# Kernel optimization log

Measured on AMD Instinct MI355X. Metric: run time of the kernel, lower is better.

## Reference

```python
import jax, jax.numpy as jnp
import numpy as np

NUM_CLASSES = 4
SMOOTH = 1e-05
W_DICE, W_CE, W_BOUND = 1.0, 1.0, 0.01
BIG = 1e8  # effectively-infinite squared distance


def _edt_sq_pass(f, axis):
    # Exact 1D squared-distance transform along `axis` via min-plus:
    # out[i] = min_j f[j] + (i-j)^2  (brute-force O(n^2), fully vectorized)
    n = f.shape[axis]
    i = jnp.arange(n, dtype=f.dtype)
    d2 = (i[:, None] - i[None, :]) ** 2  # [n, n]
    fm = jnp.moveaxis(f, axis, -1)
    out = jnp.min(fm[..., None, :] + d2, axis=-1)
    return jnp.moveaxis(out, -1, axis)


def _edt(zero_mask):
    # Euclidean distance to the nearest True voxel of zero_mask
    # (equivalent to scipy distance_transform_edt(~zero_mask)'s convention:
    #  distance to nearest zero of the input == nearest True of zero_mask).
    f = jnp.where(zero_mask, 0.0, BIG).astype(jnp.float32)
    for ax in range(f.ndim):
        f = _edt_sq_pass(f, ax)
    return jnp.sqrt(f)


def _signed_distance(mask):
    # mask: bool [D,H,W]; signed distance map: + outside, - inside.
    d_out = _edt(mask)            # distance(1 - mask)
    d_in = _edt(~mask)            # distance(mask)
    sdf = d_out - d_in
    total = jnp.sum(mask)
    size = mask.size
    sdf = jnp.where(total == 0, jnp.ones_like(sdf), sdf)
    sdf = jnp.where(total == size, -jnp.ones_like(sdf), sdf)
    return sdf


def setup_inputs() -> dict:
    key = jax.random.key(0)
    k1, k2 = jax.random.split(key)
    preds = jax.random.normal(k1, (4, NUM_CLASSES, 64, 64, 64), dtype=jnp.float32)
    targets = jax.random.randint(k2, (4, 64, 64, 64), 0, NUM_CLASSES, dtype=jnp.int32)
    return {"preds": preds, "targets": targets}


def reference(preds, targets):
    B = preds.shape[0]
    probs = jax.nn.softmax(preds, axis=1)  # [B,C,D,H,W]

    # --- Soft Dice ---
    onehot = jax.nn.one_hot(targets, NUM_CLASSES, dtype=preds.dtype)  # [B,D,H,W,C]
    onehot = jnp.moveaxis(onehot, -1, 1)  # [B,C,D,H,W]
    inter = jnp.sum(probs * onehot, axis=(2, 3, 4))
    union = jnp.sum(probs, axis=(2, 3, 4)) + jnp.sum(onehot, axis=(2, 3, 4))
    dice = (2.0 * inter + SMOOTH) / (union + SMOOTH)
    l_dice = 1.0 - jnp.mean(dice)

    # --- Cross entropy (mean over all voxels) ---
    logp = jax.nn.log_softmax(preds, axis=1)
    picked = jnp.take_along_axis(logp, targets[:, None].astype(jnp.int32), axis=1)
    l_ce = -jnp.mean(picked)

    # --- Boundary loss (classes 1..C-1) ---
    l_bound = jnp.float32(0.0)
    for c in range(1, NUM_CLASSES):
        mask_c = targets == c  # [B,D,H,W]
        sdf_c = jax.vmap(_signed_distance)(mask_c)  # [B,D,H,W]
        l_bound = l_bound + jnp.sum(jnp.mean(sdf_c * probs[:, c], axis=(1, 2, 3)))
    l_bound = l_bound / (B * (NUM_CLASSES - 1))

    return W_DICE * l_dice + W_CE * l_ce + W_BOUND * l_bound
```

## Files before the change

### kernel.cpp

```cpp
#include <hip/hip_runtime.h>
#include <hip/hip_bf16.h>
#include <math.h>

#define NVOX 262144
#define BIGF 1e8f
#define GRID_B 768
#define GRID_K2 768

__device__ __forceinline__ unsigned short f2bf(float x) {
    __hip_bfloat16 h = __float2bfloat16(x);
    return *reinterpret_cast<unsigned short*>(&h);
}
__device__ __forceinline__ float bf2f(unsigned short u) {
    __hip_bfloat16 h = *reinterpret_cast<__hip_bfloat16*>(&u);
    return __bfloat162float(h);
}
__device__ __forceinline__ unsigned short dist2_u16(unsigned long long mask, int w) {
    if (mask == 0ull) return 0xFFFFu;
    unsigned long long mr = mask >> w;
    unsigned long long ml = mask << (63 - w);
    int dr = mr ? __builtin_ctzll(mr) : 127;
    int dl = ml ? __builtin_clzll(ml) : 127;
    int dd = dr < dl ? dr : dl;
    return (unsigned short)(dd * dd);
}

__global__ __launch_bounds__(256) void kA_probs(
    const float* __restrict__ preds, unsigned short* __restrict__ probsT) {
    int bid = blockIdx.x, t = threadIdx.x;
    int g0 = bid * 1024 + 4 * t;
    int b = g0 >> 18;
    int v0 = g0 & (NVOX - 1);
    const float* p = preds + (size_t)(b * 4) * NVOX + v0;
    float4 x0 = *(const float4*)(p);
    float4 x1 = *(const float4*)(p + NVOX);
    float4 x2 = *(const float4*)(p + 2 * NVOX);
    float4 x3 = *(const float4*)(p + 3 * NVOX);

    const float L2E = 1.4426950408889634f;
    unsigned short pb[3][4];
    #pragma unroll
    for (int j = 0; j < 4; ++j) {
        float a0 = (&x0.x)[j], a1 = (&x1.x)[j], a2 = (&x2.x)[j], a3 = (&x3.x)[j];
        float m  = fmaxf(fmaxf(a0, a1), fmaxf(a2, a3));
        float e0 = exp2f((a0 - m) * L2E);
        float e1 = exp2f((a1 - m) * L2E);
        float e2 = exp2f((a2 - m) * L2E);
        float e3 = exp2f((a3 - m) * L2E);
        float inv = __builtin_amdgcn_rcpf(e0 + e1 + e2 + e3);
        pb[0][j] = f2bf(e1 * inv);
        pb[1][j] = f2bf(e2 * inv);
        pb[2][j] = f2bf(e3 * inv);
    }
    int d = v0 >> 12, h = (v0 >> 6) & 63, w0 = v0 & 63;
    size_t poff = (size_t)h * 4096 + d * 64 + w0;
    #pragma unroll
    for (int c = 0; c < 3; ++c) {
        ushort4 u = make_ushort4(pb[c][0], pb[c][1], pb[c][2], pb[c][3]);
        *(ushort4*)(probsT + (size_t)(b * 3 + c) * NVOX + poff) = u;
    }
}

__global__ __launch_bounds__(256) void kA_stats(
    const float* __restrict__ preds, const int* __restrict__ targets,
    float* __restrict__ part_stats) {
    __shared__ float sred[4 * 13];
    int bid = blockIdx.x, t = threadIdx.x, lane = t & 63, wid = t >> 6;
    int g0 = bid * 1024 + 4 * t;
    int b = g0 >> 18;
    int v0 = g0 & (NVOX - 1);
    const float* p = preds + (size_t)(b * 4) * NVOX + v0;
    float4 x0 = *(const float4*)(p);
    float4 x1 = *(const float4*)(p + NVOX);
    float4 x2 = *(const float4*)(p + 2 * NVOX);
    float4 x3 = *(const float4*)(p + 3 * NVOX);
    int4 tv4 = *(const int4*)(targets + (size_t)b * NVOX + v0);

    const float L2E = 1.4426950408889634f;
    const float LN2 = 0.6931471805599453f;
    float q[13];
    #pragma unroll
    for (int k = 0; k < 13; ++k) q[k] = 0.0f;

    #pragma unroll
    for (int j = 0; j < 4; ++j) {
        float a0 = (&x0.x)[j], a1 = (&x1.x)[j], a2 = (&x2.x)[j], a3 = (&x3.x)[j];
        int tv = (&tv4.x)[j];
        float m  = fmaxf(fmaxf(a0, a1), fmaxf(a2, a3));
        float e0 = exp2f((a0 - m) * L2E);
        float e1 = exp2f((a1 - m) * L2E);
        float e2 = exp2f((a2 - m) * L2E);
        float e3 = exp2f((a3 - m) * L2E);
        float ssum = e0 + e1 + e2 + e3;
        float inv  = __builtin_amdgcn_rcpf(ssum);
        float p0 = e0 * inv, p1 = e1 * inv, p2 = e2 * inv, p3 = e3 * inv;
        float xt = (tv == 0) ? a0 : (tv == 1) ? a1 : (tv == 2) ? a2 : a3;
        q[12] += (m - xt) + log2f(ssum) * LN2;
        q[4] += p0; q[5] += p1; q[6] += p2; q[7] += p3;
        if (tv == 0)      { q[0] += p0; q[8]  += 1.0f; }
        else if (tv == 1) { q[1] += p1; q[9]  += 1.0f; }
        else if (tv == 2) { q[2] += p2; q[10] += 1.0f; }
        else              { q[3] += p3; q[11] += 1.0f; }
    }

    #pragma unroll
    for (int k = 0; k < 13; ++k) {
        float x = q[k];
        #pragma unroll
        for (int o = 32; o > 0; o >>= 1) x += __shfl_down(x, o);
        if (lane == 0) sred[wid * 13 + k] = x;
    }
    __syncthreads();
    if (t < 13) {
        float s = sred[t] + sred[13 + t] + sred[26 + t] + sred[39 + t];
        part_stats[t * 1024 + bid] = s;
    }
}

__global__ __launch_bounds__(256) void kB_edt12(
    const int* __restrict__ targets, unsigned short* __restrict__ bufA) {
    __shared__ unsigned short tO[64 * 66];
    __shared__ unsigned short tI[64 * 66];
    int blk = blockIdx.x;
    int cm = blk % 3;
    int bd = blk / 3;
    int d = bd & 63, b = bd >> 6;
    int c = cm + 1;
    int t = threadIdx.x, lane = t & 63, wid = t >> 6;
    const int* tg = targets + (size_t)b * NVOX + (size_t)d * 4096;

    #pragma unroll
    for (int i = 0; i < 16; ++i) {
        int e = t + 256 * i;
        int h = wid + 4 * i;
        int tv = tg[e];
        unsigned long long mask = __ballot(tv == c);
        tO[h * 66 + lane] = dist2_u16(mask, lane);
        tI[h * 66 + lane] = dist2_u16(~mask, lane);
    }
    __syncthreads();

    for (int r = 0; r < 16; ++r) {
        int w = wid * 16 + r;
        {
            float best = (float)tO[lane * 66 + w];
            for (int dk = 1; dk < 64; ++dk) {
                float d2 = (float)(dk * dk);
                if (__all(d2 >= best)) break;
                int hl = lane - dk; hl = hl < 0 ? 0 : hl;
                int hr = lane + dk; hr = hr > 63 ? 63 : hr;
                best = fminf(fminf(best, (float)tO[hl * 66 + w] + d2),
                             (float)tO[hr * 66 + w] + d2);
            }
            tO[lane * 66 + w] = (unsigned short)best;
        }
        {
            float best = (float)tI[lane * 66 + w];
            for (int dk = 1; dk < 64; ++dk) {
                float d2 = (float)(dk * dk);
                if (__all(d2 >= best)) break;
                int hl = lane - dk; hl = hl < 0 ? 0 : hl;
                int hr = lane + dk; hr = hr > 63 ? 63 : hr;
                best = fminf(fminf(best, (float)tI[hl * 66 + w] + d2),
                             (float)tI[hr * 66 + w] + d2);
            }
            tI[lane * 66 + w] = (unsigned short)best;
        }
    }
    __syncthreads();

    int combo = b * 3 + cm;
    size_t oO = (size_t)combo * NVOX + (size_t)d * 64;
    size_t oI = (size_t)(combo + 12) * NVOX + (size_t)d * 64;
    #pragma unroll
    for (int i = 0; i < 16; ++i) {
        int h = wid + 4 * i;
        bufA[oO + (size_t)h * 4096 + lane] = tO[h * 66 + lane];
        bufA[oI + (size_t)h * 4096 + lane] = tI[h * 66 + lane];
    }
}

__global__ __launch_bounds__(512) void K2_edt3_sdf(
    const unsigned short* __restrict__ bufA, const unsigned short* __restrict__ probsT,
    float* __restrict__ part_bound) {
    __shared__ float pl[2][64 * 65];
    __shared__ float sredb[8];
    int blk = blockIdx.x;
    int combo = blk >> 6, h = blk & 63;
    int t = threadIdx.x, lane = t & 63, wid = t >> 6;

    for (int v = 0; v < 2; ++v) {
        const unsigned short* src = bufA + (size_t)(combo + 12 * v) * NVOX + (size_t)h * 4096;
        #pragma unroll
        for (int i = 0; i < 8; ++i) {
            int e = t + 512 * i;
            pl[v][e + (e >> 6)] = (float)src[e];
        }
    }
    __syncthreads();

    for (int v = 0; v < 2; ++v) {
        for (int r = 0; r < 8; ++r) {
            int w = wid * 8 + r;
            float* col = &pl[v][w];
            float best = col[lane * 65];
            for (int dk = 1; dk < 64; ++dk) {
                float d2 = (float)(dk * dk);
                if (__all(d2 >= best)) break;
                int dl = lane - dk; dl = dl < 0 ? 0 : dl;
                int dr = lane + dk; dr = dr > 63 ? 63 : dr;
                best = fminf(fminf(best, col[dl * 65] + d2), col[dr * 65] + d2);
            }
            col[lane * 65] = best;
        }
    }
    __syncthreads();

    const unsigned short* pp = probsT + (size_t)combo * NVOX + (size_t)h * 4096;
    float acc = 0.0f;
    #pragma unroll
    for (int i = 0; i < 8; ++i) {
        int e = t + 512 * i;
        int li = e + (e >> 6);
        float sdf = sqrtf(pl[0][li]) - sqrtf(pl[1][li]);
        acc += sdf * bf2f(pp[e]);
    }
    #pragma unroll
    for (int o = 32; o > 0; o >>= 1) acc += __shfl_down(acc, o);
    if (lane == 0) sredb[wid] = acc;
    __syncthreads();
    if (t == 0) {
        float s = 0.0f;
        for (int j = 0; j < 8; ++j) s += sredb[j];
        part_bound[blk] = s;
    }
}

__global__ __launch_bounds__(1024) void K3_final(
    const float* __restrict__ part_stats, const float* __restrict__ part_bound,
    float* __restrict__ out) {
    __shared__ float sred[13 * 16];
    __shared__ float bred[12];
    __shared__ double S[52];
    int t = threadIdx.x, lane = t & 63, wid = t >> 6;

    float v[13];
    #pragma unroll
    for (int k = 0; k < 13; ++k) v[k] = part_stats[k * 1024 + t];
    float bv = (wid < 12) ? part_bound[wid * 64 + lane] : 0.0f;

    #pragma unroll
    for (int k = 0; k < 13; ++k) {
        float x = v[k];
        #pragma unroll
        for (int o = 32; o > 0; o >>= 1) x += __shfl_down(x, o);
        if (lane == 0) sred[k * 16 + wid] = x;
    }
    #pragma unroll
    for (int o = 32; o > 0; o >>= 1) bv += __shfl_down(bv, o);
    if (lane == 0 && wid < 12) bred[wid] = bv;
    __syncthreads();

    if (t < 52) {
        int k = t >> 2, b = t & 3;
        S[k * 4 + b] = (double)sred[k * 16 + b * 4]     + (double)sred[k * 16 + b * 4 + 1]
                     + (double)sred[k * 16 + b * 4 + 2] + (double)sred[k * 16 + b * 4 + 3];
    }
    __syncthreads();
    if (t == 0) {
        const double NV = (double)NVOX;
        double dice_sum = 0.0;
        for (int b = 0; b < 4; ++b)
            for (int c = 0; c < 4; ++c) {
                double inter = S[c * 4 + b];
                double un    = S[(4 + c) * 4 + b] + S[(8 + c) * 4 + b];
                dice_sum += (2.0 * inter + 1e-5) / (un + 1e-5);
            }
        double l_dice = 1.0 - dice_sum / 16.0;
        double l_ce = (S[48] + S[49] + S[50] + S[51]) / (4.0 * NV);
        double lb = 0.0;
        for (int cb = 0; cb < 12; ++cb) {
            int b = cb / 3, c = cb % 3 + 1;
            double cnt = S[(8 + c) * 4 + b];
            double s;
            if (cnt == 0.0)      s =  S[(4 + c) * 4 + b];
            else if (cnt == NV)  s = -S[(4 + c) * 4 + b];
            else                 s =  (double)bred[cb];
            lb += s / NV;
        }
        lb /= 12.0;
        out[0] = (float)(l_dice + l_ce + 0.01 * lb);
    }
}

extern "C" void kernel_launch(void* const* d_in, const int* in_sizes, int n_in,
                              void* d_out, int out_size, void* d_ws, size_t ws_size,
                              hipStream_t stream) {
    const float* preds   = (const float*)d_in[0];
    const int*   targets = (const int*)d_in[1];
    float* out = (float*)d_out;

    unsigned short* bufA   = (unsigned short*)d_ws;
    unsigned short* probsT = bufA + (size_t)24 * NVOX;
    float* part_stats = (float*)(probsT + (size_t)12 * NVOX);
    float* part_bound = part_stats + 13 * 1024;

    kA_probs<<<1024, 256, 0, stream>>>(preds, probsT);
    kA_stats<<<1024, 256, 0, stream>>>(preds, targets, part_stats);
    kB_edt12<<<GRID_B, 256, 0, stream>>>(targets, bufA);
    K2_edt3_sdf<<<GRID_K2, 512, 0, stream>>>(bufA, probsT, part_bound);
    K3_final<<<1, 1024, 0, stream>>>(part_stats, part_bound, out);
}
```

Before: 56.46 us.

## Fuse softmax stats and probability computation into the third EDT pass kernel

Removes the separate softmax-probability and statistics kernels and the bf16 transposed probability buffer. The third-axis EDT kernel now runs one block per (batch, h) slab, handles all three classes' inside/outside tiles in shared memory, and computes softmax, dice, CE stats and boundary sums in registers. It also switches the min-plus passes from float to unsigned integer arithmetic and drops bf16 storage of probs. Grid shrinks from 768 to 256 blocks with larger shared memory per block, which may lower occupancy and parallelism.

After: 54.02 us. 1.05x faster.

```diff
diff --git a/kernel.cpp b/kernel.cpp
--- a/kernel.cpp
+++ b/kernel.cpp
@@ -1,20 +1,9 @@
 #include <hip/hip_runtime.h>
-#include <hip/hip_bf16.h>
 #include <math.h>
 
 #define NVOX 262144
-#define BIGF 1e8f
 #define GRID_B 768
-#define GRID_K2 768
-
-__device__ __forceinline__ unsigned short f2bf(float x) {
-    __hip_bfloat16 h = __float2bfloat16(x);
-    return *reinterpret_cast<unsigned short*>(&h);
-}
-__device__ __forceinline__ float bf2f(unsigned short u) {
-    __hip_bfloat16 h = *reinterpret_cast<__hip_bfloat16*>(&u);
-    return __bfloat162float(h);
-}
+
 __device__ __forceinline__ unsigned short dist2_u16(unsigned long long mask, int w) {
     if (mask == 0ull) return 0xFFFFu;
     unsigned long long mr = mask >> w;
@@ -23,98 +12,6 @@
     int dl = ml ? __builtin_clzll(ml) : 127;
     int dd = dr < dl ? dr : dl;
     return (unsigned short)(dd * dd);
-}
-
-__global__ __launch_bounds__(256) void kA_probs(
-    const float* __restrict__ preds, unsigned short* __restrict__ probsT) {
-    int bid = blockIdx.x, t = threadIdx.x;
-    int g0 = bid * 1024 + 4 * t;
-    int b = g0 >> 18;
-    int v0 = g0 & (NVOX - 1);
-    const float* p = preds + (size_t)(b * 4) * NVOX + v0;
-    float4 x0 = *(const float4*)(p);
-    float4 x1 = *(const float4*)(p + NVOX);
-    float4 x2 = *(const float4*)(p + 2 * NVOX);
-    float4 x3 = *(const float4*)(p + 3 * NVOX);
-
-    const float L2E = 1.4426950408889634f;
-    unsigned short pb[3][4];
-    #pragma unroll
-    for (int j = 0; j < 4; ++j) {
-        float a0 = (&x0.x)[j], a1 = (&x1.x)[j], a2 = (&x2.x)[j], a3 = (&x3.x)[j];
-        float m  = fmaxf(fmaxf(a0, a1), fmaxf(a2, a3));
-        float e0 = exp2f((a0 - m) * L2E);
-        float e1 = exp2f((a1 - m) * L2E);
-        float e2 = exp2f((a2 - m) * L2E);
-        float e3 = exp2f((a3 - m) * L2E);
-        float inv = __builtin_amdgcn_rcpf(e0 + e1 + e2 + e3);
-        pb[0][j] = f2bf(e1 * inv);
-        pb[1][j] = f2bf(e2 * inv);
-        pb[2][j] = f2bf(e3 * inv);
-    }
-    int d = v0 >> 12, h = (v0 >> 6) & 63, w0 = v0 & 63;
-    size_t poff = (size_t)h * 4096 + d * 64 + w0;
-    #pragma unroll
-    for (int c = 0; c < 3; ++c) {
-        ushort4 u = make_ushort4(pb[c][0], pb[c][1], pb[c][2], pb[c][3]);
-        *(ushort4*)(probsT + (size_t)(b * 3 + c) * NVOX + poff) = u;
-    }
-}
-
-__global__ __launch_bounds__(256) void kA_stats(
-    const float* __restrict__ preds, const int* __restrict__ targets,
-    float* __restrict__ part_stats) {
-    __shared__ float sred[4 * 13];
-    int bid = blockIdx.x, t = threadIdx.x, lane = t & 63, wid = t >> 6;
-    int g0 = bid * 1024 + 4 * t;
-    int b = g0 >> 18;
-    int v0 = g0 & (NVOX - 1);
-    const float* p = preds + (size_t)(b * 4) * NVOX + v0;
-    float4 x0 = *(const float4*)(p);
-    float4 x1 = *(const float4*)(p + NVOX);
-    float4 x2 = *(const float4*)(p + 2 * NVOX);
-    float4 x3 = *(const float4*)(p + 3 * NVOX);
-    int4 tv4 = *(const int4*)(targets + (size_t)b * NVOX + v0);
-
-    const float L2E = 1.4426950408889634f;
-    const float LN2 = 0.6931471805599453f;
-    float q[13];
-    #pragma unroll
-    for (int k = 0; k < 13; ++k) q[k] = 0.0f;
-
-    #pragma unroll
-    for (int j = 0; j < 4; ++j) {
-        float a0 = (&x0.x)[j], a1 = (&x1.x)[j], a2 = (&x2.x)[j], a3 = (&x3.x)[j];
-        int tv = (&tv4.x)[j];
-        float m  = fmaxf(fmaxf(a0, a1), fmaxf(a2, a3));
-        float e0 = exp2f((a0 - m) * L2E);
-        float e1 = exp2f((a1 - m) * L2E);
-        float e2 = exp2f((a2 - m) * L2E);
-        float e3 = exp2f((a3 - m) * L2E);
-        float ssum = e0 + e1 + e2 + e3;
-        float inv  = __builtin_amdgcn_rcpf(ssum);
-        float p0 = e0 * inv, p1 = e1 * inv, p2 = e2 * inv, p3 = e3 * inv;
-        float xt = (tv == 0) ? a0 : (tv == 1) ? a1 : (tv == 2) ? a2 : a3;
-        q[12] += (m - xt) + log2f(ssum) * LN2;
-        q[4] += p0; q[5] += p1; q[6] += p2; q[7] += p3;
-        if (tv == 0)      { q[0] += p0; q[8]  += 1.0f; }
-        else if (tv == 1) { q[1] += p1; q[9]  += 1.0f; }
-        else if (tv == 2) { q[2] += p2; q[10] += 1.0f; }
-        else              { q[3] += p3; q[11] += 1.0f; }
-    }
-
-    #pragma unroll
-    for (int k = 0; k < 13; ++k) {
-        float x = q[k];
-        #pragma unroll
-        for (int o = 32; o > 0; o >>= 1) x += __shfl_down(x, o);
-        if (lane == 0) sred[wid * 13 + k] = x;
-    }
-    __syncthreads();
-    if (t < 13) {
-        float s = sred[t] + sred[13 + t] + sred[26 + t] + sred[39 + t];
-        part_stats[t * 1024 + bid] = s;
-    }
 }
 
 __global__ __launch_bounds__(256) void kB_edt12(
@@ -143,26 +40,30 @@
     for (int r = 0; r < 16; ++r) {
         int w = wid * 16 + r;
         {
-            float best = (float)tO[lane * 66 + w];
+            unsigned best = tO[lane * 66 + w];
             for (int dk = 1; dk < 64; ++dk) {
-                float d2 = (float)(dk * dk);
+                unsigned d2 = (unsigned)(dk * dk);
                 if (__all(d2 >= best)) break;
                 int hl = lane - dk; hl = hl < 0 ? 0 : hl;
                 int hr = lane + dk; hr = hr > 63 ? 63 : hr;
-                best = fminf(fminf(best, (float)tO[hl * 66 + w] + d2),
-                             (float)tO[hr * 66 + w] + d2);
+                unsigned ca = tO[hl * 66 + w] + d2;
+                unsigned cb = tO[hr * 66 + w] + d2;
+                ca = ca < cb ? ca : cb;
+                best = best < ca ? best : ca;
             }
             tO[lane * 66 + w] = (unsigned short)best;
         }
         {
-            float best = (float)tI[lane * 66 + w];
+            unsigned best = tI[lane * 66 + w];
             for (int dk = 1; dk < 64; ++dk) {
-                float d2 = (float)(dk * dk);
+                unsigned d2 = (unsigned)(dk * dk);
                 if (__all(d2 >= best)) break;
                 int hl = lane - dk; hl = hl < 0 ? 0 : hl;
                 int hr = lane + dk; hr = hr > 63 ? 63 : hr;
-                best = fminf(fminf(best, (float)tI[hl * 66 + w] + d2),
-                             (float)tI[hr * 66 + w] + d2);
+                unsigned ca = tI[hl * 66 + w] + d2;
+                unsigned cb = tI[hr * 66 + w] + d2;
+                ca = ca < cb ? ca : cb;
+                best = best < ca ? best : ca;
             }
             tI[lane * 66 + w] = (unsigned short)best;
         }
@@ -180,92 +81,161 @@
     }
 }
 
-__global__ __launch_bounds__(512) void K2_edt3_sdf(
-    const unsigned short* __restrict__ bufA, const unsigned short* __restrict__ probsT,
-    float* __restrict__ part_bound) {
-    __shared__ float pl[2][64 * 65];
-    __shared__ float sredb[8];
+__global__ __launch_bounds__(512) void K2_big(
+    const float* __restrict__ preds, const int* __restrict__ targets,
+    unsigned short* __restrict__ bufA,
+    float* __restrict__ part_stats, float* __restrict__ part_bound) {
+    __shared__ unsigned short tile[6][64 * 66];
+    __shared__ float sred[8][16];
+    __shared__ float bsum[8][3];
     int blk = blockIdx.x;
-    int combo = blk >> 6, h = blk & 63;
+    int b = blk >> 6, h = blk & 63;
     int t = threadIdx.x, lane = t & 63, wid = t >> 6;
 
-    for (int v = 0; v < 2; ++v) {
-        const unsigned short* src = bufA + (size_t)(combo + 12 * v) * NVOX + (size_t)h * 4096;
-        #pragma unroll
-        for (int i = 0; i < 8; ++i) {
-            int e = t + 512 * i;
-            pl[v][e + (e >> 6)] = (float)src[e];
-        }
-    }
-    __syncthreads();
-
-    for (int v = 0; v < 2; ++v) {
-        for (int r = 0; r < 8; ++r) {
-            int w = wid * 8 + r;
-            float* col = &pl[v][w];
-            float best = col[lane * 65];
-            for (int dk = 1; dk < 64; ++dk) {
-                float d2 = (float)(dk * dk);
-                if (__all(d2 >= best)) break;
-                int dl = lane - dk; dl = dl < 0 ? 0 : dl;
-                int dr = lane + dk; dr = dr > 63 ? 63 : dr;
-                best = fminf(fminf(best, col[dl * 65] + d2), col[dr * 65] + d2);
-            }
-            col[lane * 65] = best;
-        }
-    }
-    __syncthreads();
-
-    const unsigned short* pp = probsT + (size_t)combo * NVOX + (size_t)h * 4096;
-    float acc = 0.0f;
-    #pragma unroll
-    for (int i = 0; i < 8; ++i) {
-        int e = t + 512 * i;
-        int li = e + (e >> 6);
-        float sdf = sqrtf(pl[0][li]) - sqrtf(pl[1][li]);
-        acc += sdf * bf2f(pp[e]);
-    }
-    #pragma unroll
-    for (int o = 32; o > 0; o >>= 1) acc += __shfl_down(acc, o);
-    if (lane == 0) sredb[wid] = acc;
-    __syncthreads();
-    if (t == 0) {
+    int e0 = 8 * t, d0 = e0 >> 6, w0 = e0 & 63;
+    #pragma unroll
+    for (int p = 0; p < 6; ++p) {
+        int cm = p >> 1, v = p & 1;
+        const unsigned short* src =
+            bufA + (size_t)(b * 3 + cm + 12 * v) * NVOX + (size_t)h * 4096 + e0;
+        uint4 u = *(const uint4*)src;
+        unsigned* dst32 = (unsigned*)&tile[p][d0 * 66 + w0];
+        dst32[0] = u.x; dst32[1] = u.y; dst32[2] = u.z; dst32[3] = u.w;
+    }
+
+    size_t vbase = (size_t)d0 * 4096 + (size_t)h * 64 + w0;
+    const float* pp = preds + (size_t)(b * 4) * NVOX + vbase;
+    float4 f[4][2];
+    #pragma unroll
+    for (int c = 0; c < 4; ++c) {
+        f[c][0] = *(const float4*)(pp + (size_t)c * NVOX);
+        f[c][1] = *(const float4*)(pp + (size_t)c * NVOX + 4);
+    }
+    const int* tp = targets + (size_t)b * NVOX + vbase;
+    int4 tg0 = *(const int4*)(tp);
+    int4 tg1 = *(const int4*)(tp + 4);
+
+    const float L2E = 1.4426950408889634f;
+    const float LN2 = 0.6931471805599453f;
+    float q[13];
+    #pragma unroll
+    for (int k = 0; k < 13; ++k) q[k] = 0.0f;
+    float pr[3][8];
+
+    #pragma unroll
+    for (int j = 0; j < 8; ++j) {
+        float a0 = (&f[0][j >> 2].x)[j & 3];
+        float a1 = (&f[1][j >> 2].x)[j & 3];
+        float a2 = (&f[2][j >> 2].x)[j & 3];
+        float a3 = (&f[3][j >> 2].x)[j & 3];
+        int tv = (j < 4) ? (&tg0.x)[j] : (&tg1.x)[j - 4];
+        float m  = fmaxf(fmaxf(a0, a1), fmaxf(a2, a3));
+        float e0_ = exp2f((a0 - m) * L2E);
+        float e1_ = exp2f((a1 - m) * L2E);
+        float e2_ = exp2f((a2 - m) * L2E);
+        float e3_ = exp2f((a3 - m) * L2E);
+        float ssum = e0_ + e1_ + e2_ + e3_;
+        float inv  = __builtin_amdgcn_rcpf(ssum);
+        float p0 = e0_ * inv, p1 = e1_ * inv, p2 = e2_ * inv, p3 = e3_ * inv;
+        float xt = (tv == 0) ? a0 : (tv == 1) ? a1 : (tv == 2) ? a2 : a3;
+        q[12] += (m - xt) + log2f(ssum) * LN2;
+        q[4] += p0; q[5] += p1; q[6] += p2; q[7] += p3;
+        if (tv == 0)      { q[0] += p0; q[8]  += 1.0f; }
+        else if (tv == 1) { q[1] += p1; q[9]  += 1.0f; }
+        else if (tv == 2) { q[2] += p2; q[10] += 1.0f; }
+        else              { q[3] += p3; q[11] += 1.0f; }
+        pr[0][j] = p1; pr[1][j] = p2; pr[2][j] = p3;
+    }
+    __syncthreads();
+
+    for (int job = wid; job < 384; job += 8) {
+        int p = job >> 6, w = job & 63;
+        unsigned short* T = tile[p];
+        unsigned best = T[lane * 66 + w];
+        for (int dk = 1; dk < 64; ++dk) {
+            unsigned d2 = (unsigned)(dk * dk);
+            if (__all(d2 >= best)) break;
+            int dl = lane - dk; dl = dl < 0 ? 0 : dl;
+            int dr = lane + dk; dr = dr > 63 ? 63 : dr;
+            unsigned ca = T[dl * 66 + w] + d2;
+            unsigned cb = T[dr * 66 + w] + d2;
+            ca = ca < cb ? ca : cb;
+            best = best < ca ? best : ca;
+        }
+        T[lane * 66 + w] = (unsigned short)best;
+    }
+    __syncthreads();
+
+    float accb[3] = {0.0f, 0.0f, 0.0f};
+    #pragma unroll
+    for (int j = 0; j < 8; ++j) {
+        int idx = d0 * 66 + w0 + j;
+        #pragma unroll
+        for (int cm = 0; cm < 3; ++cm) {
+            float dO = (float)tile[2 * cm][idx];
+            float dI = (float)tile[2 * cm + 1][idx];
+            float sdf = sqrtf(dO) - sqrtf(dI);
+            accb[cm] += sdf * pr[cm][j];
+        }
+    }
+
+    #pragma unroll
+    for (int k = 0; k < 13; ++k) {
+        float x = q[k];
+        #pragma unroll
+        for (int o = 32; o > 0; o >>= 1) x += __shfl_down(x, o);
+        if (lane == 0) sred[wid][k] = x;
+    }
+    #pragma unroll
+    for (int cm = 0; cm < 3; ++cm) {
+        float x = accb[cm];
+        #pragma unroll
+        for (int o = 32; o > 0; o >>= 1) x += __shfl_down(x, o);
+        if (lane == 0) bsum[wid][cm] = x;
+    }
+    __syncthreads();
+    if (t < 13) {
         float s = 0.0f;
-        for (int j = 0; j < 8; ++j) s += sredb[j];
-        part_bound[blk] = s;
+        #pragma unroll
+        for (int ww = 0; ww < 8; ++ww) s += sred[ww][t];
+        part_stats[t * 256 + blk] = s;
+    }
+    if (t >= 64 && t < 67) {
+        int cm = t - 64;
+        float s = 0.0f;
+        #pragma unroll
+        for (int ww = 0; ww < 8; ++ww) s += bsum[ww][cm];
+        part_bound[(b * 3 + cm) * 64 + h] = s;
     }
 }
 
 __global__ __launch_bounds__(1024) void K3_final(
     const float* __restrict__ part_stats, const float* __restrict__ part_bound,
     float* __restrict__ out) {
-    __shared__ float sred[13 * 16];
+    __shared__ float sred[52];
     __shared__ float bred[12];
     __shared__ double S[52];
     int t = threadIdx.x, lane = t & 63, wid = t >> 6;
 
-    float v[13];
-    #pragma unroll
-    for (int k = 0; k < 13; ++k) v[k] = part_stats[k * 1024 + t];
-    float bv = (wid < 12) ? part_bound[wid * 64 + lane] : 0.0f;
-
-    #pragma unroll
-    for (int k = 0; k < 13; ++k) {
-        float x = v[k];
-        #pragma unroll
-        for (int o = 32; o > 0; o >>= 1) x += __shfl_down(x, o);
-        if (lane == 0) sred[k * 16 + wid] = x;
-    }
-    #pragma unroll
-    for (int o = 32; o > 0; o >>= 1) bv += __shfl_down(bv, o);
-    if (lane == 0 && wid < 12) bred[wid] = bv;
-    __syncthreads();
-
-    if (t < 52) {
-        int k = t >> 2, b = t & 3;
-        S[k * 4 + b] = (double)sred[k * 16 + b * 4]     + (double)sred[k * 16 + b * 4 + 1]
-                     + (double)sred[k * 16 + b * 4 + 2] + (double)sred[k * 16 + b * 4 + 3];
-    }
+    if (wid < 4) {
+        float v[13];
+        #pragma unroll
+        for (int k = 0; k < 13; ++k) v[k] = part_stats[k * 256 + t];
+        #pragma unroll
+        for (int k = 0; k < 13; ++k) {
+            float x = v[k];
+            #pragma unroll
+            for (int o = 32; o > 0; o >>= 1) x += __shfl_down(x, o);
+            if (lane == 0) sred[k * 4 + wid] = x;
+        }
+    } else {
+        float bv = part_bound[(wid - 4) * 64 + lane];
+        #pragma unroll
+        for (int o = 32; o > 0; o >>= 1) bv += __shfl_down(bv, o);
+        if (lane == 0) bred[wid - 4] = bv;
+    }
+    __syncthreads();
+    if (t < 52) S[t] = (double)sred[t];
     __syncthreads();
     if (t == 0) {
         const double NV = (double)NVOX;
@@ -300,14 +270,11 @@
     const int*   targets = (const int*)d_in[1];
     float* out = (float*)d_out;
 
-    unsigned short* bufA   = (unsigned short*)d_ws;
-    unsigned short* probsT = bufA + (size_t)24 * NVOX;
-    float* part_stats = (float*)(probsT + (size_t)12 * NVOX);
-    float* part_bound = part_stats + 13 * 1024;
-
-    kA_probs<<<1024, 256, 0, stream>>>(preds, probsT);
-    kA_stats<<<1024, 256, 0, stream>>>(preds, targets, part_stats);
+    unsigned short* bufA = (unsigned short*)d_ws;
+    float* part_stats = (float*)(bufA + (size_t)24 * NVOX);
+    float* part_bound = part_stats + 13 * 256;
+
     kB_edt12<<<GRID_B, 256, 0, stream>>>(targets, bufA);
-    K2_edt3_sdf<<<GRID_K2, 512, 0, stream>>>(bufA, probsT, part_bound);
+    K2_big<<<256, 512, 0, stream>>>(preds, targets, bufA, part_stats, part_bound);
     K3_final<<<1, 1024, 0, stream>>>(part_stats, part_bound, out);
 }
```
